# Kernel optimization log

Hardware: AMD Instinct MI355X
Metric: run time of the kernel (lower is better)

The kernel has to match this reference:

```python
import jax, jax.numpy as jnp
import numpy as np

K = 3
STRIDE = 1
PAD = 1


def conv2d(x, w, b, stride=1, padding=0):
    out = jax.lax.conv_general_dilated(
        x, w, (stride, stride), [(padding, padding), (padding, padding)],
        dimension_numbers=('NCHW', 'OIHW', 'NCHW'))
    return out + b[None, :, None, None]


def setup_inputs() -> dict:
    key = jax.random.key(0)
    ks = jax.random.split(key, 12)
    n, m, k = 64, 64, K
    sc = 0.05
    inp = {
        'x': jax.random.normal(ks[0], (8, n, 128, 128), jnp.float32),
        # attention1: Conv(n->k^2, k, s, p), Conv(k^2->k^2, 1), Conv(k^2->k^2, 1)
        'a1w1': jax.random.normal(ks[1], (k * k, n, k, k), jnp.float32) * sc,
        'a1b1': jax.random.normal(ks[2], (k * k,), jnp.float32) * sc,
        'a1w2': jax.random.normal(ks[3], (k * k, k * k, 1, 1), jnp.float32) * sc,
        'a1b2': jax.random.normal(ks[4], (k * k,), jnp.float32) * sc,
        'a1w3': jax.random.normal(ks[5], (k * k, k * k, 1, 1), jnp.float32) * sc,
        'a1b3': jax.random.normal(ks[6], (k * k,), jnp.float32) * sc,
        # attention3 (dynamic bias): Conv(n->m,1), Conv(m->m,1) after global avg pool
        'a3w1': jax.random.normal(ks[7], (m, n, 1, 1), jnp.float32) * sc,
        'a3b1': jax.random.normal(ks[8], (m,), jnp.float32) * sc,
        'a3w2': jax.random.normal(ks[9], (m, m, 1, 1), jnp.float32) * sc,
        'a3b2': jax.random.normal(ks[10], (m,), jnp.float32) * sc,
        # main conv weight (m, n, k, k)
        'weight': jax.random.normal(ks[11], (m, n, k, k), jnp.float32) * sc,
    }
    return inp


def reference(x, a1w1, a1b1, a1w2, a1b2, a1w3, a1b3, a3w1, a3b1, a3w2, a3b2, weight):
    k, s, p = K, STRIDE, PAD
    b, n, H, W = x.shape
    m = weight.shape[0]
    # per-pixel kernel attention: (b, k^2, nH, nW) in ki*k+kj order
    a = jax.nn.relu(conv2d(x, a1w1, a1b1, s, p))
    a = jax.nn.relu(conv2d(a, a1w2, a1b2))
    atw = jax.nn.sigmoid(conv2d(a, a1w3, a1b3))
    # im2col: (b, n*k^2, nH, nW), channel-major (c, ki, kj) like torch.unfold
    patches = jax.lax.conv_general_dilated_patches(
        x, (k, k), (s, s), [(p, p), (p, p)],
        dimension_numbers=('NCHW', 'OIHW', 'NCHW'))
    _, _, nH, nW = patches.shape
    patches = patches.reshape(b, n, k * k, nH, nW)
    # attention weights are repeated across input channels (the .repeat in torch)
    atx = patches * atw[:, None]                      # (b, n, k2, nH, nW)
    w = weight.reshape(m, n, k * k)
    y = jnp.einsum('bnpij,mnp->bmij', atx, w)          # (b, m, nH, nW)
    # dynamic bias from global average pool
    g = jnp.mean(x, axis=(2, 3), keepdims=True)        # (b, n, 1, 1)
    bias = conv2d(jax.nn.relu(conv2d(g, a3w1, a3b1)), a3w2, a3b2)  # (b, m, 1, 1)
    return y + bias
```

## Files before the change

kernel.cpp:

```cpp
#include <hip/hip_runtime.h>
#include <hip/hip_bf16.h>
#include <math.h>

#define HW 128
#define NPIX (HW * HW)
#define NB 8
#define PH 130
#define PPIX (PH * PH)

#define HC3 34
#define NPXT3 (4 * HC3)
#define NCHUNK (NPXT3 * 8)

typedef __attribute__((ext_vector_type(8))) short bf16x8;
typedef __attribute__((ext_vector_type(4))) float f32x4;
typedef __attribute__((ext_vector_type(16))) float f32x16;

static __device__ __forceinline__ short f2bf(float v) {
  union { float f; unsigned u; } a; a.f = v;
  unsigned r = a.u + 0x7fffu + ((a.u >> 16) & 1u);
  return (short)(r >> 16);
}
static __device__ __forceinline__ float bfbits2f(unsigned u) {
  union { unsigned u; float f; } a; a.u = u; return a.f;
}
static __device__ __forceinline__ unsigned pkbf2(float lo, float hi) {
  __hip_bfloat162 pk = __float22bfloat162_rn(make_float2(lo, hi));
  union { __hip_bfloat162 h; unsigned u; } cv; cv.h = pk;
  return cv.u;
}

__global__ __launch_bounds__(256) void k_pack(const float* __restrict__ wgt,
                                              const float* __restrict__ a1w1,
                                              short* __restrict__ Apack,
                                              short* __restrict__ A1pack,
                                              short* __restrict__ xT) {
  int bx = blockIdx.x;
  if (bx < 144) {
    int idx = bx * 256 + threadIdx.x;
    if (idx < 9 * 64 * 64) {
      int p = idx >> 12, m = (idx >> 6) & 63, n = idx & 63;
      Apack[idx] = f2bf(wgt[(m * 64 + n) * 9 + p]);
    }
    if (idx < 9 * 16 * 64) {
      int p = idx >> 10, q = (idx >> 6) & 15, n = idx & 63;
      A1pack[idx] = (q < 9) ? f2bf(a1w1[(q * 64 + n) * 9 + p]) : (short)0;
    }
  } else {
    int b = bx - 144;
    for (int c = threadIdx.x; c < 4128; c += 256) {
      int i = c >> 3, q = c & 7;
      int gpix;
      if (i < 130) gpix = i;
      else if (i < 260) gpix = 129 * 130 + (i - 130);
      else { int j = i - 260; gpix = (1 + (j >> 1)) * PH + ((j & 1) ? 129 : 0); }
      *(uint4*)(xT + ((size_t)b * PPIX + gpix) * 64 + q * 8) = make_uint4(0, 0, 0, 0);
    }
  }
}

__global__ __launch_bounds__(256) void k_tr(const float* __restrict__ x,
                                            short* __restrict__ xT) {
  int b = blockIdx.y;
  int tid = threadIdx.x;
  int pix = (blockIdx.x << 8) + tid;
  const float* xb = x + (size_t)b * 64 * NPIX + pix;
  unsigned pk[32];
  #pragma unroll
  for (int cp = 0; cp < 32; cp++) {
    float v0 = xb[(size_t)(2 * cp) * NPIX];
    float v1 = xb[(size_t)(2 * cp + 1) * NPIX];
    pk[cp] = pkbf2(v0, v1);
  }
  int row = pix >> 7, col = pix & 127;
  short* dst = xT + ((size_t)b * PPIX + (size_t)(row + 1) * PH + (col + 1)) * 64;
  #pragma unroll
  for (int q = 0; q < 8; q++)
    *(uint4*)(dst + q * 8) =
        make_uint4(pk[4 * q], pk[4 * q + 1], pk[4 * q + 2], pk[4 * q + 3]);
}

__global__ __launch_bounds__(256) void k_gpool2(const short* __restrict__ xT,
                                                float* __restrict__ part) {
  int b = blockIdx.y, strip = blockIdx.x;
  int tid = threadIdx.x;
  int wid = tid >> 6, lane = tid & 63;
  int q = tid & 7, slot = tid >> 3;
  const short* xb = xT + (size_t)b * PPIX * 64;
  float s[8];
  #pragma unroll
  for (int k = 0; k < 8; k++) s[k] = 0.f;
  #pragma unroll 4
  for (int itr = 0; itr < 64; itr++) {
    int px = strip * 2048 + itr * 32 + slot;
    int r = px >> 7, c = px & 127;
    uint4 v = *(const uint4*)(xb + ((size_t)((r + 1) * PH + c + 1)) * 64 + q * 8);
    s[0] += bfbits2f(v.x << 16); s[1] += bfbits2f(v.x & 0xffff0000u);
    s[2] += bfbits2f(v.y << 16); s[3] += bfbits2f(v.y & 0xffff0000u);
    s[4] += bfbits2f(v.z << 16); s[5] += bfbits2f(v.z & 0xffff0000u);
    s[6] += bfbits2f(v.w << 16); s[7] += bfbits2f(v.w & 0xffff0000u);
  }
  #pragma unroll
  for (int o = 8; o < 64; o <<= 1)
    #pragma unroll
    for (int k = 0; k < 8; k++) s[k] += __shfl_down(s[k], o, 64);
  __shared__ float red[4][64];
  if (lane < 8) {
    #pragma unroll
    for (int k = 0; k < 8; k++) red[wid][lane * 8 + k] = s[k];
  }
  __syncthreads();
  if (tid < 64)
    part[((size_t)b * 8 + strip) * 64 + tid] =
        red[0][tid] + red[1][tid] + red[2][tid] + red[3][tid];
}

__global__ __launch_bounds__(64) void k_bias(const float* __restrict__ part,
                                             const float* __restrict__ a3w1,
                                             const float* __restrict__ a3b1,
                                             const float* __restrict__ a3w2,
                                             const float* __restrict__ a3b2,
                                             float* __restrict__ bias) {
  int b = blockIdx.x;
  int t = threadIdx.x;
  __shared__ float gsh[64], h[64];
  float gs = 0.f;
  #pragma unroll
  for (int sIdx = 0; sIdx < 8; sIdx++) gs += part[((size_t)b * 8 + sIdx) * 64 + t];
  gsh[t] = gs * (1.0f / NPIX);
  __syncthreads();
  float s1 = a3b1[t];
  #pragma unroll
  for (int n = 0; n < 64; n++) s1 += a3w1[t * 64 + n] * gsh[n];
  h[t] = fmaxf(s1, 0.f);
  __syncthreads();
  float s2 = a3b2[t];
  #pragma unroll
  for (int c = 0; c < 64; c++) s2 += a3w2[t * 64 + c] * h[c];
  bias[b * 64 + t] = s2;
}

__global__ __launch_bounds__(256, 4) void k_fused(
    const short* __restrict__ xT, const short* __restrict__ Apack,
    const short* __restrict__ A1pack,
    const float* __restrict__ b1p, const float* __restrict__ w2p,
    const float* __restrict__ b2p, const float* __restrict__ w3p,
    const float* __restrict__ b3p,
    const float* __restrict__ bias, float* __restrict__ out) {
  __shared__ short xt[NPXT3 * 64];

  int b = blockIdx.y;
  int ty = blockIdx.x >> 2, tx = blockIdx.x & 3;
  int row0 = ty * 2, col0 = tx * 32;

  int tid = threadIdx.x;
  int wid = tid >> 6, lane = tid & 63;
  int lp = lane & 15, kq = lane >> 4;
  int ml = lane & 31, kh = lane >> 5;
  int wr = wid >> 1;
  int m0 = (wid & 1) * 32;

  {
    const short* xTb = xT + (size_t)b * PPIX * 64;
    int base = row0 * PH + col0;
    for (int c = tid; c < NCHUNK; c += 256) {
      int pix = c >> 3;
      int r = pix / HC3, col = pix - r * HC3;
      bf16x8 v = *(const bf16x8*)(xTb + (size_t)(base + r * PH + col) * 64 + (c & 7) * 8);
      *(bf16x8*)((char*)xt + ((c * 16) ^ ((pix & 7) << 4))) = v;
    }
  }
  __syncthreads();

  f32x4 acc1[2];
  acc1[0] = acc1[1] = (f32x4){0.f, 0.f, 0.f, 0.f};
  #pragma unroll
  for (int p = 0; p < 9; p++) {
    const int di = p / 3, dj = p % 3;
    #pragma unroll
    for (int ck = 0; ck < 2; ck++) {
      bf16x8 af1 = *(const bf16x8*)(A1pack + (p * 16 + lp) * 64 + ck * 32 + kq * 8);
      #pragma unroll
      for (int g = 0; g < 2; g++) {
        int pix = (wr + di) * HC3 + g * 16 + dj + lp;
        int byteoff = (pix * 128 + ck * 64 + kq * 16) ^ ((pix & 7) << 4);
        bf16x8 bf = *(const bf16x8*)((const char*)xt + byteoff);
        acc1[g] = __builtin_amdgcn_mfma_f32_16x16x32_bf16(af1, bf, acc1[g], 0, 0, 0);
      }
    }
  }

  float aw[2][9];
  #pragma unroll
  for (int g = 0; g < 2; g++) {
    float a[9], t1[9], t2[9];
    #pragma unroll
    for (int q2 = 0; q2 < 9; q2++)
      a[q2] = __shfl(acc1[g][q2 & 3], (q2 >> 2) * 16 + lp, 64);
    #pragma unroll
    for (int q = 0; q < 9; q++) t1[q] = fmaxf(a[q] + b1p[q], 0.f);
    #pragma unroll
    for (int r = 0; r < 9; r++) {
      float s = b2p[r];
      #pragma unroll
      for (int q = 0; q < 9; q++) s += w2p[r * 9 + q] * t1[q];
      t2[r] = fmaxf(s, 0.f);
    }
    #pragma unroll
    for (int r = 0; r < 9; r++) {
      float s = b3p[r];
      #pragma unroll
      for (int q = 0; q < 9; q++) s += w3p[r * 9 + q] * t2[q];
      aw[g][r] = 1.f / (1.f + __expf(-s));
    }
  }
  float aw9[9];
  #pragma unroll
  for (int p = 0; p < 9; p++) aw9[p] = (lane & 16) ? aw[1][p] : aw[0][p];

  f32x16 acc;
  #pragma unroll
  for (int r = 0; r < 16; r++) acc[r] = 0.f;

  #pragma unroll
  for (int p = 0; p < 9; p++) {
    const int di = p / 3, dj = p % 3;
    int pixb = (wr + di) * HC3 + dj + ml;
    bf16x8 af[4], fr[4];
    #pragma unroll
    for (int ck = 0; ck < 4; ck++) {
      af[ck] = *(const bf16x8*)(Apack + ((size_t)(p * 64 + m0 + ml)) * 64 + ck * 16 + kh * 8);
      int byteoff = (pixb * 128 + ck * 32 + kh * 16) ^ ((pixb & 7) << 4);
      fr[ck] = *(const bf16x8*)((const char*)xt + byteoff);
    }
    f32x16 tmp;
    #pragma unroll
    for (int r = 0; r < 16; r++) tmp[r] = 0.f;
    #pragma unroll
    for (int ck = 0; ck < 4; ck++)
      tmp = __builtin_amdgcn_mfma_f32_32x32x16_bf16(af[ck], fr[ck], tmp, 0, 0, 0);
    float awp = aw9[p];
    #pragma unroll
    for (int r = 0; r < 16; r++) acc[r] += awp * tmp[r];
  }

  int i = row0 + wr;
  #pragma unroll
  for (int q = 0; q < 4; q++) {
    f32x4 bv = *(const f32x4*)(bias + b * 64 + m0 + q * 8 + kh * 4);
    #pragma unroll
    for (int rr = 0; rr < 3 + 1; rr++) {
      int m = m0 + rr + q * 8 + kh * 4;
      out[(((size_t)b * 64 + m) * HW + i) * HW + col0 + ml] = acc[q * 4 + rr] + bv[rr];
    }
  }
}

extern "C" void kernel_launch(void* const* d_in, const int* in_sizes, int n_in,
                              void* d_out, int out_size, void* d_ws, size_t ws_size,
                              hipStream_t stream) {
  const float* x    = (const float*)d_in[0];
  const float* a1w1 = (const float*)d_in[1];
  const float* a1b1 = (const float*)d_in[2];
  const float* a1w2 = (const float*)d_in[3];
  const float* a1b2 = (const float*)d_in[4];
  const float* a1w3 = (const float*)d_in[5];
  const float* a1b3 = (const float*)d_in[6];
  const float* a3w1 = (const float*)d_in[7];
  const float* a3b1 = (const float*)d_in[8];
  const float* a3w2 = (const float*)d_in[9];
  const float* a3b2 = (const float*)d_in[10];
  const float* wgt  = (const float*)d_in[11];
  float* out = (float*)d_out;

  const size_t xT_sh = (size_t)NB * PPIX * 64;
  short* xT     = (short*)d_ws;
  float* part   = (float*)(xT + xT_sh);
  float* bias   = part + NB * 8 * 64;
  short* Apack  = (short*)(bias + NB * 64);
  short* A1pack = Apack + 9 * 64 * 64;

  k_pack<<<dim3(152), dim3(256), 0, stream>>>(wgt, a1w1, Apack, A1pack, xT);
  k_tr<<<dim3(64, NB), dim3(256), 0, stream>>>(x, xT);
  k_gpool2<<<dim3(8, NB), dim3(256), 0, stream>>>(xT, part);
  k_bias<<<dim3(NB), dim3(64), 0, stream>>>(part, a3w1, a3b1, a3w2, a3b2, bias);
  k_fused<<<dim3(256, NB), dim3(256), 0, stream>>>(xT, Apack, A1pack,
                                                   a1b1, a1w2, a1b2, a1w3, a1b3,
                                                   bias, out);
}
```

Baseline: 97.87 us.

## Read input tiles directly from global memory and compute attention MLP once per lane

```diff
diff --git a/kernel.cpp b/kernel.cpp
--- a/kernel.cpp
+++ b/kernel.cpp
@@ -7,10 +7,6 @@
 #define NB 8
 #define PH 130
 #define PPIX (PH * PH)
-
-#define HC3 34
-#define NPXT3 (4 * HC3)
-#define NCHUNK (NPXT3 * 8)
 
 typedef __attribute__((ext_vector_type(8))) short bf16x8;
 typedef __attribute__((ext_vector_type(4))) float f32x4;
@@ -147,30 +143,21 @@
     const float* __restrict__ b2p, const float* __restrict__ w3p,
     const float* __restrict__ b3p,
     const float* __restrict__ bias, float* __restrict__ out) {
-  __shared__ short xt[NPXT3 * 64];
-
   int b = blockIdx.y;
-  int ty = blockIdx.x >> 2, tx = blockIdx.x & 3;
-  int row0 = ty * 2, col0 = tx * 32;
+  int bx = blockIdx.x;
+  int i = bx >> 1;
+  int half = bx & 1;
 
   int tid = threadIdx.x;
   int wid = tid >> 6, lane = tid & 63;
   int lp = lane & 15, kq = lane >> 4;
   int ml = lane & 31, kh = lane >> 5;
-  int wr = wid >> 1;
-  int m0 = (wid & 1) * 32;
-
-  {
-    const short* xTb = xT + (size_t)b * PPIX * 64;
-    int base = row0 * PH + col0;
-    for (int c = tid; c < NCHUNK; c += 256) {
-      int pix = c >> 3;
-      int r = pix / HC3, col = pix - r * HC3;
-      bf16x8 v = *(const bf16x8*)(xTb + (size_t)(base + r * PH + col) * 64 + (c & 7) * 8);
-      *(bf16x8*)((char*)xt + ((c * 16) ^ ((pix & 7) << 4))) = v;
-    }
-  }
-  __syncthreads();
+  int col0 = half * 64 + (wid & 1) * 32;
+  int m0 = (wid >> 1) * 32;
+
+  const short* xTb = xT + (size_t)b * PPIX * 64;
+  int prow = i;
+  int pcol = col0;
 
   f32x4 acc1[2];
   acc1[0] = acc1[1] = (f32x4){0.f, 0.f, 0.f, 0.f};
@@ -182,21 +169,24 @@
       bf16x8 af1 = *(const bf16x8*)(A1pack + (p * 16 + lp) * 64 + ck * 32 + kq * 8);
       #pragma unroll
       for (int g = 0; g < 2; g++) {
-        int pix = (wr + di) * HC3 + g * 16 + dj + lp;
-        int byteoff = (pix * 128 + ck * 64 + kq * 16) ^ ((pix & 7) << 4);
-        bf16x8 bf = *(const bf16x8*)((const char*)xt + byteoff);
+        int pp = (prow + di) * PH + pcol + g * 16 + lp + dj;
+        bf16x8 bf = *(const bf16x8*)(xTb + (size_t)pp * 64 + ck * 32 + kq * 8);
         acc1[g] = __builtin_amdgcn_mfma_f32_16x16x32_bf16(af1, bf, acc1[g], 0, 0, 0);
       }
     }
   }
 
-  float aw[2][9];
-  #pragma unroll
-  for (int g = 0; g < 2; g++) {
+  int gme = (lane >> 4) & 1;
+  float aw9[9];
+  {
     float a[9], t1[9], t2[9];
     #pragma unroll
-    for (int q2 = 0; q2 < 9; q2++)
-      a[q2] = __shfl(acc1[g][q2 & 3], (q2 >> 2) * 16 + lp, 64);
+    for (int q2 = 0; q2 < 9; q2++) {
+      int src = (q2 >> 2) * 16 + lp;
+      float lo = __shfl(acc1[0][q2 & 3], src, 64);
+      float hi = __shfl(acc1[1][q2 & 3], src, 64);
+      a[q2] = gme ? hi : lo;
+    }
     #pragma unroll
     for (int q = 0; q < 9; q++) t1[q] = fmaxf(a[q] + b1p[q], 0.f);
     #pragma unroll
@@ -211,12 +201,9 @@
       float s = b3p[r];
       #pragma unroll
       for (int q = 0; q < 9; q++) s += w3p[r * 9 + q] * t2[q];
-      aw[g][r] = 1.f / (1.f + __expf(-s));
-    }
-  }
-  float aw9[9];
-  #pragma unroll
-  for (int p = 0; p < 9; p++) aw9[p] = (lane & 16) ? aw[1][p] : aw[0][p];
+      aw9[r] = 1.f / (1.f + __expf(-s));
+    }
+  }
 
   f32x16 acc;
   #pragma unroll
@@ -225,13 +212,12 @@
   #pragma unroll
   for (int p = 0; p < 9; p++) {
     const int di = p / 3, dj = p % 3;
-    int pixb = (wr + di) * HC3 + dj + ml;
+    int pp = (prow + di) * PH + pcol + ml + dj;
     bf16x8 af[4], fr[4];
     #pragma unroll
     for (int ck = 0; ck < 4; ck++) {
       af[ck] = *(const bf16x8*)(Apack + ((size_t)(p * 64 + m0 + ml)) * 64 + ck * 16 + kh * 8);
-      int byteoff = (pixb * 128 + ck * 32 + kh * 16) ^ ((pixb & 7) << 4);
-      fr[ck] = *(const bf16x8*)((const char*)xt + byteoff);
+      fr[ck] = *(const bf16x8*)(xTb + (size_t)pp * 64 + ck * 16 + kh * 8);
     }
     f32x16 tmp;
     #pragma unroll
@@ -244,12 +230,11 @@
     for (int r = 0; r < 16; r++) acc[r] += awp * tmp[r];
   }
 
-  int i = row0 + wr;
   #pragma unroll
   for (int q = 0; q < 4; q++) {
     f32x4 bv = *(const f32x4*)(bias + b * 64 + m0 + q * 8 + kh * 4);
     #pragma unroll
-    for (int rr = 0; rr < 3 + 1; rr++) {
+    for (int rr = 0; rr < 4; rr++) {
       int m = m0 + rr + q * 8 + kh * 4;
       out[(((size_t)b * 64 + m) * HW + i) * HW + col0 + ml] = acc[q * 4 + rr] + bv[rr];
     }
```

After: 150.8 us. 1.54x slower.
